# Optimization experiments

Measured on AMD Instinct MI355X. Metric: run time of the kernel, lower is better.

Reference implementation:

```python
import jax, jax.numpy as jnp
import numpy as np

N_NODES = 100000


def gcn_conv(x, edge_index, W, b, n_nodes):
    """PyG GCNConv: add self-loops, symmetric deg^-1/2 normalization,
    linear transform, scatter-add aggregate, bias."""
    src, dst = edge_index[0], edge_index[1]
    # add self-loops
    loop = jnp.arange(n_nodes, dtype=edge_index.dtype)
    src = jnp.concatenate([src, loop])
    dst = jnp.concatenate([dst, loop])
    # transform first (in_dim >= out_dim ordering used by PyG)
    h = x @ W  # [N, out]
    # symmetric normalization from in-degree (incl. self-loops)
    ones = jnp.ones(src.shape[0], dtype=x.dtype)
    deg = jax.ops.segment_sum(ones, dst, num_segments=n_nodes)
    dinv = jnp.where(deg > 0, jax.lax.rsqrt(deg), 0.0).astype(x.dtype)
    norm = dinv[src] * dinv[dst]  # [E+N]
    msg = h[src] * norm[:, None]  # gather + scale
    out = jax.ops.segment_sum(msg, dst, num_segments=n_nodes)
    return out + b


def setup_inputs() -> dict:
    key = jax.random.key(0)
    k1, k2, k3, k4 = jax.random.split(key, 4)
    n, e = N_NODES, 1600000
    d_in, d_hid, n_cls = 256, 256, 64
    x = jax.random.normal(k1, (n, d_in), dtype=jnp.float32)
    edge_index = jax.random.randint(k2, (2, e), 0, n, dtype=jnp.int64)
    W1 = jax.random.normal(k3, (d_in, d_hid), dtype=jnp.float32) / np.sqrt(d_in)
    b1 = jnp.zeros((d_hid,), dtype=jnp.float32)
    W2 = jax.random.normal(k4, (d_hid, n_cls), dtype=jnp.float32) / np.sqrt(d_hid)
    b2 = jnp.zeros((n_cls,), dtype=jnp.float32)
    return {"x": x, "edge_index": edge_index, "W1": W1, "b1": b1, "W2": W2, "b2": b2}


def reference(x, edge_index, W1, b1, W2, b2):
    n = x.shape[0]
    h = jax.nn.relu(gcn_conv(x, edge_index, W1, b1, n))
    # dropout is identity in eval mode (training=False)
    logits = gcn_conv(h, edge_index, W2, b2, n)
    return jax.nn.log_softmax(logits, axis=1)
```

## Files before the change

kernel.cpp:

```cpp
#include <hip/hip_runtime.h>
#include <math.h>


typedef __attribute__((ext_vector_type(8))) short bf16x8;
typedef __attribute__((ext_vector_type(4))) float f32x4;

__device__ inline unsigned short f2bf(float f) {
    union { float f; unsigned int u; } v; v.f = f;
    unsigned int r = v.u + 0x7fffu + ((v.u >> 16) & 1u);
    return (unsigned short)(r >> 16);
}
__device__ inline float bf2f_lo(unsigned int u) {
    union { unsigned int u; float f; } v; v.u = u << 16; return v.f;
}
__device__ inline float bf2f_hi(unsigned int u) {
    union { unsigned int u; float f; } v; v.u = u & 0xffff0000u; return v.f;
}

__device__ inline void acc8(float* acc, uint4 q, float w) {
    acc[0] += bf2f_lo(q.x) * w; acc[1] += bf2f_hi(q.x) * w;
    acc[2] += bf2f_lo(q.y) * w; acc[3] += bf2f_hi(q.y) * w;
    acc[4] += bf2f_lo(q.z) * w; acc[5] += bf2f_hi(q.z) * w;
    acc[6] += bf2f_lo(q.w) * w; acc[7] += bf2f_hi(q.w) * w;
}

__global__ __launch_bounds__(256) void deg_rank_kernel(
    const int* __restrict__ dst, int E, int* __restrict__ cnt,
    int* __restrict__ rank) {
    int e = blockIdx.x * blockDim.x + threadIdx.x;
    if (e < E) rank[e] = atomicAdd(&cnt[dst[e]], 1);
}

__global__ __launch_bounds__(256) void scan_part1_kernel(
    const int* __restrict__ cnt, int* __restrict__ bsum, int N) {
    __shared__ int s[256];
    const int tid = threadIdx.x;
    int base = blockIdx.x * 1024 + tid * 4;
    int v = 0;
#pragma unroll
    for (int j = 0; j < 4; ++j)
        if (base + j < N) v += cnt[base + j];
    s[tid] = v;
    __syncthreads();
    for (int off = 128; off > 0; off >>= 1) {
        if (tid < off) s[tid] += s[tid + off];
        __syncthreads();
    }
    if (tid == 0) bsum[blockIdx.x] = s[0];
}

__global__ __launch_bounds__(1024) void scan_part2_kernel(
    const int* __restrict__ bsum, int* __restrict__ boffs, int NB,
    int* __restrict__ row_ptr, int N) {
    __shared__ int s[1024];
    const int tid = threadIdx.x;
    int v = (tid < NB) ? bsum[tid] : 0;
    s[tid] = v;
    __syncthreads();
    for (int off = 1; off < 1024; off <<= 1) {
        int t = (tid >= off) ? s[tid - off] : 0;
        __syncthreads();
        if (tid >= off) s[tid] += t;
        __syncthreads();
    }
    if (tid < NB) boffs[tid] = s[tid] - v;
    if (tid == 1023) row_ptr[N] = s[1023];
}

__global__ __launch_bounds__(256) void scan_part3_kernel(
    const int* __restrict__ cnt, const int* __restrict__ boffs,
    int* __restrict__ row_ptr, int N) {
    __shared__ int s[256];
    const int tid = threadIdx.x;
    int base = blockIdx.x * 1024 + tid * 4;
    int c[4];
    int v = 0;
#pragma unroll
    for (int j = 0; j < 4; ++j) {
        c[j] = (base + j < N) ? cnt[base + j] : 0;
        v += c[j];
    }
    s[tid] = v;
    __syncthreads();
    for (int off = 1; off < 256; off <<= 1) {
        int t = (tid >= off) ? s[tid - off] : 0;
        __syncthreads();
        if (tid >= off) s[tid] += t;
        __syncthreads();
    }
    int run = boffs[blockIdx.x] + s[tid] - v;
#pragma unroll
    for (int j = 0; j < 4; ++j) {
        if (base + j < N) {
            row_ptr[base + j] = run;
            run += c[j];
        }
    }
}

__global__ __launch_bounds__(256) void scatter_kernel(
    const int* __restrict__ src, const int* __restrict__ dst,
    const int* __restrict__ rank, const int* __restrict__ cnt,
    const int* __restrict__ row_ptr, int2* __restrict__ csr_ew, int E) {
    int e = blockIdx.x * blockDim.x + threadIdx.x;
    if (e >= E) return;
    int s = src[e], d = dst[e];
    float w = rsqrtf((float)cnt[s] + 1.0f) * rsqrtf((float)cnt[d] + 1.0f);
    int pos = row_ptr[d] + rank[e];
    int2 rec;
    rec.x = s;
    rec.y = __float_as_int(w);
    csr_ew[pos] = rec;
}

__global__ __launch_bounds__(256) void castw_kernel(
    const float* __restrict__ W1, const float* __restrict__ W2,
    unsigned short* __restrict__ W1t, unsigned short* __restrict__ W2t) {
    int i = blockIdx.x * 256 + threadIdx.x;
    if (i < 65536) {
        int n = i >> 8, k = i & 255;
        W1t[i] = f2bf(W1[(size_t)k * 256 + n]);
    } else if (i < 65536 + 16384) {
        int j = i - 65536;
        int n = j >> 8, k = j & 255;
        W2t[j] = f2bf(W2[(size_t)k * 64 + n]);
    }
}

__global__ __launch_bounds__(256) void gemm1_kernel(
    const float* __restrict__ A, const unsigned short* __restrict__ Bt,
    unsigned short* __restrict__ C, int M) {
    __shared__ unsigned short As[128][32];
    __shared__ unsigned short Bs[256][32];

    const int tid = threadIdx.x;
    const int wave = tid >> 6, lane = tid & 63;
    const int quad = lane >> 4, l15 = lane & 15;
    const int m0 = blockIdx.x * 128;

    f32x4 acc[8][4] = {};

    const int arow = tid >> 1;
    const int akk  = (tid & 1) << 4;
    const int gr = m0 + arow;

    for (int k0 = 0; k0 < 256; k0 += 32) {
        float4 a0 = make_float4(0.f,0.f,0.f,0.f), a1 = a0, a2 = a0, a3 = a0;
        if (gr < M) {
            const float* ap = &A[(size_t)gr * 256 + k0 + akk];
            a0 = *(const float4*)&ap[0];
            a1 = *(const float4*)&ap[4];
            a2 = *(const float4*)&ap[8];
            a3 = *(const float4*)&ap[12];
        }
        bf16x8 av0, av1;
        av0[0] = (short)f2bf(a0.x); av0[1] = (short)f2bf(a0.y);
        av0[2] = (short)f2bf(a0.z); av0[3] = (short)f2bf(a0.w);
        av0[4] = (short)f2bf(a1.x); av0[5] = (short)f2bf(a1.y);
        av0[6] = (short)f2bf(a1.z); av0[7] = (short)f2bf(a1.w);
        av1[0] = (short)f2bf(a2.x); av1[1] = (short)f2bf(a2.y);
        av1[2] = (short)f2bf(a2.z); av1[3] = (short)f2bf(a2.w);
        av1[4] = (short)f2bf(a3.x); av1[5] = (short)f2bf(a3.y);
        av1[6] = (short)f2bf(a3.z); av1[7] = (short)f2bf(a3.w);
        *(bf16x8*)&As[arow][akk]     = av0;
        *(bf16x8*)&As[arow][akk + 8] = av1;

        const unsigned short* bsrc = &Bt[(size_t)tid * 256 + k0];
        *(bf16x8*)&Bs[tid][0]  = *(const bf16x8*)&bsrc[0];
        *(bf16x8*)&Bs[tid][8]  = *(const bf16x8*)&bsrc[8];
        *(bf16x8*)&Bs[tid][16] = *(const bf16x8*)&bsrc[16];
        *(bf16x8*)&Bs[tid][24] = *(const bf16x8*)&bsrc[24];
        __syncthreads();

        bf16x8 bfv[4];
#pragma unroll
        for (int nt = 0; nt < 4; ++nt)
            bfv[nt] = *(const bf16x8*)&Bs[wave * 64 + nt * 16 + l15][quad * 8];
#pragma unroll
        for (int mt = 0; mt < 8; ++mt) {
            bf16x8 af = *(const bf16x8*)&As[mt * 16 + l15][quad * 8];
#pragma unroll
            for (int nt = 0; nt < 4; ++nt)
                acc[mt][nt] = __builtin_amdgcn_mfma_f32_16x16x32_bf16(
                    af, bfv[nt], acc[mt][nt], 0, 0, 0);
        }
        __syncthreads();
    }

#pragma unroll
    for (int mt = 0; mt < 8; ++mt) {
#pragma unroll
        for (int nt = 0; nt < 4; ++nt) {
            int gcol = wave * 64 + nt * 16 + l15;
#pragma unroll
            for (int r = 0; r < 4; ++r) {
                int grow = m0 + mt * 16 + quad * 4 + r;
                if (grow < M)
                    C[(size_t)grow * 256 + gcol] = f2bf(acc[mt][nt][r]);
            }
        }
    }
}

__global__ __launch_bounds__(256) void agg256b_kernel(
    const uint4* __restrict__ h,
    const int2* __restrict__ ew,
    const int* __restrict__ row_ptr, const int* __restrict__ cnt,
    const float* __restrict__ bias, uint4* __restrict__ outb, int N) {
    const int node = blockIdx.x * 4 + (threadIdx.x >> 6);
    if (node >= N) return;
    const int lane = threadIdx.x & 63;
    const int half = lane >> 5;
    const int c = lane & 31;

    float dv = rsqrtf((float)cnt[node] + 1.0f);
    float w0 = dv * dv;

    float acc[8] = {0.f, 0.f, 0.f, 0.f, 0.f, 0.f, 0.f, 0.f};
    {
        uint4 q = h[(size_t)node * 32 + c];
        acc8(acc, q, half == 0 ? w0 : 0.f);
    }

    const int beg = row_ptr[node], end = row_ptr[node + 1];
    int e = beg;
    for (; e + 8 <= end; e += 8) {
        int2 r0 = ew[e + 0 + half];
        int2 r1 = ew[e + 2 + half];
        int2 r2 = ew[e + 4 + half];
        int2 r3 = ew[e + 6 + half];
        uint4 q0 = h[(size_t)r0.x * 32 + c];
        uint4 q1 = h[(size_t)r1.x * 32 + c];
        uint4 q2 = h[(size_t)r2.x * 32 + c];
        uint4 q3 = h[(size_t)r3.x * 32 + c];
        acc8(acc, q0, __int_as_float(r0.y));
        acc8(acc, q1, __int_as_float(r1.y));
        acc8(acc, q2, __int_as_float(r2.y));
        acc8(acc, q3, __int_as_float(r3.y));
    }
    for (; e < end; e += 2) {
        int idx = e + half;
        int idxc = min(idx, end - 1);
        int2 r = ew[idxc];
        float w = (idx < end) ? __int_as_float(r.y) : 0.f;
        uint4 q = h[(size_t)r.x * 32 + c];
        acc8(acc, q, w);
    }

#pragma unroll
    for (int k = 0; k < 8; ++k) acc[k] += __shfl_xor(acc[k], 32, 64);

    if (half == 0) {
        float4 b0 = *(const float4*)&bias[c * 8];
        float4 b1 = *(const float4*)&bias[c * 8 + 4];
        unsigned int o0 = f2bf(fmaxf(acc[0] + b0.x, 0.f));
        unsigned int o1 = f2bf(fmaxf(acc[1] + b0.y, 0.f));
        unsigned int o2 = f2bf(fmaxf(acc[2] + b0.z, 0.f));
        unsigned int o3 = f2bf(fmaxf(acc[3] + b0.w, 0.f));
        unsigned int o4 = f2bf(fmaxf(acc[4] + b1.x, 0.f));
        unsigned int o5 = f2bf(fmaxf(acc[5] + b1.y, 0.f));
        unsigned int o6 = f2bf(fmaxf(acc[6] + b1.z, 0.f));
        unsigned int o7 = f2bf(fmaxf(acc[7] + b1.w, 0.f));
        uint4 ov;
        ov.x = o0 | (o1 << 16);
        ov.y = o2 | (o3 << 16);
        ov.z = o4 | (o5 << 16);
        ov.w = o6 | (o7 << 16);
        outb[(size_t)node * 32 + c] = ov;
    }
}

__global__ __launch_bounds__(256) void gemm2_kernel(
    const unsigned short* __restrict__ Ab, const unsigned short* __restrict__ Bt,
    unsigned short* __restrict__ C, int M) {
    __shared__ unsigned short As[64][32];
    __shared__ unsigned short Bs[64][32];

    const int tid = threadIdx.x;
    const int wave = tid >> 6, lane = tid & 63;
    const int quad = lane >> 4, l15 = lane & 15;
    const int m0 = blockIdx.x * 64;

    f32x4 acc[4] = {};

    const int arow = tid >> 2;
    const int akk = (tid & 3) << 3;
    const int gr = m0 + arow;
    const int bn = tid & 63, bkc = (tid >> 6) << 3;

    for (int k0 = 0; k0 < 256; k0 += 32) {
        bf16x8 av = {};
        if (gr < M) av = *(const bf16x8*)&Ab[(size_t)gr * 256 + k0 + akk];
        *(bf16x8*)&As[arow][akk] = av;
        *(bf16x8*)&Bs[bn][bkc] = *(const bf16x8*)&Bt[(size_t)bn * 256 + k0 + bkc];
        __syncthreads();

        bf16x8 af = *(const bf16x8*)&As[wave * 16 + l15][quad * 8];
#pragma unroll
        for (int nt = 0; nt < 4; ++nt) {
            bf16x8 bfv = *(const bf16x8*)&Bs[nt * 16 + l15][quad * 8];
            acc[nt] = __builtin_amdgcn_mfma_f32_16x16x32_bf16(af, bfv, acc[nt], 0, 0, 0);
        }
        __syncthreads();
    }

#pragma unroll
    for (int nt = 0; nt < 4; ++nt) {
#pragma unroll
        for (int r = 0; r < 4; ++r) {
            int grow = m0 + wave * 16 + quad * 4 + r;
            if (grow < M) C[(size_t)grow * 64 + nt * 16 + l15] = f2bf(acc[nt][r]);
        }
    }
}

__global__ __launch_bounds__(256) void agg64_kernel(
    const uint4* __restrict__ h,
    const int2* __restrict__ ew, const int* __restrict__ row_ptr,
    const int* __restrict__ cnt, const float* __restrict__ bias,
    float* __restrict__ out, int N) {
    const int node = blockIdx.x * 4 + (threadIdx.x >> 6);
    if (node >= N) return;
    const int lane = threadIdx.x & 63;
    const int g = lane >> 3;
    const int c = lane & 7;

    float dv = rsqrtf((float)cnt[node] + 1.0f);
    float w0 = dv * dv;

    float acc[8] = {0.f, 0.f, 0.f, 0.f, 0.f, 0.f, 0.f, 0.f};
    {
        uint4 q = h[(size_t)node * 8 + c];
        acc8(acc, q, g == 0 ? w0 : 0.f);
    }

    const int beg = row_ptr[node], end = row_ptr[node + 1];
    int e = beg;
    for (; e + 16 <= end; e += 16) {
        int2 r0 = ew[e + g];
        int2 r1 = ew[e + 8 + g];
        uint4 q0 = h[(size_t)r0.x * 8 + c];
        uint4 q1 = h[(size_t)r1.x * 8 + c];
        acc8(acc, q0, __int_as_float(r0.y));
        acc8(acc, q1, __int_as_float(r1.y));
    }
    for (; e < end; e += 8) {
        int idx = e + g;
        int idxc = min(idx, end - 1);
        int2 r = ew[idxc];
        float w = (idx < end) ? __int_as_float(r.y) : 0.f;
        uint4 q = h[(size_t)r.x * 8 + c];
        acc8(acc, q, w);
    }

#pragma unroll
    for (int k = 0; k < 8; ++k) {
        acc[k] += __shfl_xor(acc[k], 8, 64);
        acc[k] += __shfl_xor(acc[k], 16, 64);
        acc[k] += __shfl_xor(acc[k], 32, 64);
    }

    float4 b0 = *(const float4*)&bias[c * 8];
    float4 b1 = *(const float4*)&bias[c * 8 + 4];
    float v[8];
    v[0] = acc[0] + b0.x; v[1] = acc[1] + b0.y;
    v[2] = acc[2] + b0.z; v[3] = acc[3] + b0.w;
    v[4] = acc[4] + b1.x; v[5] = acc[5] + b1.y;
    v[6] = acc[6] + b1.z; v[7] = acc[7] + b1.w;

    float m = v[0];
#pragma unroll
    for (int k = 1; k < 8; ++k) m = fmaxf(m, v[k]);
    m = fmaxf(m, __shfl_xor(m, 1, 64));
    m = fmaxf(m, __shfl_xor(m, 2, 64));
    m = fmaxf(m, __shfl_xor(m, 4, 64));
    float s = 0.f;
#pragma unroll
    for (int k = 0; k < 8; ++k) s += expf(v[k] - m);
    s += __shfl_xor(s, 1, 64);
    s += __shfl_xor(s, 2, 64);
    s += __shfl_xor(s, 4, 64);
    float ls = m + logf(s);

    if (g == 0) {
        float4 o0, o1;
        o0.x = v[0] - ls; o0.y = v[1] - ls; o0.z = v[2] - ls; o0.w = v[3] - ls;
        o1.x = v[4] - ls; o1.y = v[5] - ls; o1.z = v[6] - ls; o1.w = v[7] - ls;
        *(float4*)&out[(size_t)node * 64 + c * 8] = o0;
        *(float4*)&out[(size_t)node * 64 + c * 8 + 4] = o1;
    }
}

extern "C" void kernel_launch(void* const* d_in, const int* in_sizes, int n_in,
                              void* d_out, int out_size, void* d_ws, size_t ws_size,
                              hipStream_t stream) {
    const float* x  = (const float*)d_in[0];
    const int*   ei = (const int*)d_in[1];
    const float* W1 = (const float*)d_in[2];
    const float* b1 = (const float*)d_in[3];
    const float* W2 = (const float*)d_in[4];
    const float* b2 = (const float*)d_in[5];
    float* out = (float*)d_out;

    const int N = in_sizes[0] / 256;
    const int E = in_sizes[1] / 2;
    const int NP = 102400;
    const int NB = (N + 1023) / 1024;

    char* ws = (char*)d_ws;
    int*   cnt     = (int*)ws;                 ws += (size_t)NP * 4;
    int*   rank    = (int*)ws;                 ws += (size_t)E * 4;
    int*   row_ptr = (int*)ws;                 ws += (size_t)(NP + 4) * 4;
    int*   bsum    = (int*)ws;                 ws += (size_t)1024 * 4;
    int*   boffs   = (int*)ws;                 ws += (size_t)1024 * 4;
    int2*  csr_ew  = (int2*)ws;                ws += (size_t)E * 8;
    unsigned short* W1t   = (unsigned short*)ws; ws += (size_t)256 * 256 * 2;
    unsigned short* W2t   = (unsigned short*)ws; ws += (size_t)256 * 64 * 2;
    unsigned short* h1b   = (unsigned short*)ws; ws += (size_t)N * 256 * 2;
    unsigned short* agg1b = (unsigned short*)ws; ws += (size_t)N * 256 * 2;
    unsigned short* h2b   = (unsigned short*)ws; ws += (size_t)N * 64 * 2;

    hipMemsetAsync(cnt, 0, (size_t)N * sizeof(int), stream);

    deg_rank_kernel<<<(E + 255) / 256, 256, 0, stream>>>(ei + E, E, cnt, rank);
    scan_part1_kernel<<<NB, 256, 0, stream>>>(cnt, bsum, N);
    scan_part2_kernel<<<1, 1024, 0, stream>>>(bsum, boffs, NB, row_ptr, N);
    scan_part3_kernel<<<NB, 256, 0, stream>>>(cnt, boffs, row_ptr, N);
    scatter_kernel<<<(E + 255) / 256, 256, 0, stream>>>(
        ei, ei + E, rank, cnt, row_ptr, csr_ew, E);

    castw_kernel<<<(65536 + 16384 + 255) / 256, 256, 0, stream>>>(W1, W2, W1t, W2t);

    gemm1_kernel<<<(N + 127) / 128, 256, 0, stream>>>(x, W1t, h1b, N);

    agg256b_kernel<<<(N + 3) / 4, 256, 0, stream>>>(
        (const uint4*)h1b, csr_ew, row_ptr, cnt, b1, (uint4*)agg1b, N);

    gemm2_kernel<<<(N + 63) / 64, 256, 0, stream>>>(agg1b, W2t, h2b, N);

    agg64_kernel<<<(N + 3) / 4, 256, 0, stream>>>(
        (const uint4*)h2b, csr_ew, row_ptr, cnt, b2, out, N);
}
```

Before: 554.4 us.

## Fuse layer-1 aggregation with layer-2 GEMM via shared-memory tile

The layer-1 neighbour aggregation kernel and the second GEMM become one kernel. Each block aggregates 16 nodes (4 per wave), applies bias and ReLU, stores the bf16 rows in LDS, then multiplies them by W2 with MFMA and writes h2 directly. This removes the N×256 bf16 intermediate write/read and one launch. In exchange each wave processes 4 nodes serially and W2t fragments are read from global memory per block, not staged in LDS.

```diff
diff --git a/kernel.cpp b/kernel.cpp
--- a/kernel.cpp
+++ b/kernel.cpp
@@ -202,115 +202,94 @@
     }
 }
 
-__global__ __launch_bounds__(256) void agg256b_kernel(
+__global__ __launch_bounds__(256) void aggfused_kernel(
     const uint4* __restrict__ h,
     const int2* __restrict__ ew,
     const int* __restrict__ row_ptr, const int* __restrict__ cnt,
-    const float* __restrict__ bias, uint4* __restrict__ outb, int N) {
-    const int node = blockIdx.x * 4 + (threadIdx.x >> 6);
-    if (node >= N) return;
-    const int lane = threadIdx.x & 63;
+    const float* __restrict__ bias, const unsigned short* __restrict__ W2t,
+    unsigned short* __restrict__ h2b, int N) {
+    __shared__ unsigned short As[16][264];
+
+    const int tid = threadIdx.x;
+    const int wave = tid >> 6, lane = tid & 63;
     const int half = lane >> 5;
     const int c = lane & 31;
-
-    float dv = rsqrtf((float)cnt[node] + 1.0f);
-    float w0 = dv * dv;
-
-    float acc[8] = {0.f, 0.f, 0.f, 0.f, 0.f, 0.f, 0.f, 0.f};
-    {
-        uint4 q = h[(size_t)node * 32 + c];
-        acc8(acc, q, half == 0 ? w0 : 0.f);
-    }
-
-    const int beg = row_ptr[node], end = row_ptr[node + 1];
-    int e = beg;
-    for (; e + 8 <= end; e += 8) {
-        int2 r0 = ew[e + 0 + half];
-        int2 r1 = ew[e + 2 + half];
-        int2 r2 = ew[e + 4 + half];
-        int2 r3 = ew[e + 6 + half];
-        uint4 q0 = h[(size_t)r0.x * 32 + c];
-        uint4 q1 = h[(size_t)r1.x * 32 + c];
-        uint4 q2 = h[(size_t)r2.x * 32 + c];
-        uint4 q3 = h[(size_t)r3.x * 32 + c];
-        acc8(acc, q0, __int_as_float(r0.y));
-        acc8(acc, q1, __int_as_float(r1.y));
-        acc8(acc, q2, __int_as_float(r2.y));
-        acc8(acc, q3, __int_as_float(r3.y));
-    }
-    for (; e < end; e += 2) {
-        int idx = e + half;
-        int idxc = min(idx, end - 1);
-        int2 r = ew[idxc];
-        float w = (idx < end) ? __int_as_float(r.y) : 0.f;
-        uint4 q = h[(size_t)r.x * 32 + c];
-        acc8(acc, q, w);
-    }
-
-#pragma unroll
-    for (int k = 0; k < 8; ++k) acc[k] += __shfl_xor(acc[k], 32, 64);
-
-    if (half == 0) {
-        float4 b0 = *(const float4*)&bias[c * 8];
-        float4 b1 = *(const float4*)&bias[c * 8 + 4];
-        unsigned int o0 = f2bf(fmaxf(acc[0] + b0.x, 0.f));
-        unsigned int o1 = f2bf(fmaxf(acc[1] + b0.y, 0.f));
-        unsigned int o2 = f2bf(fmaxf(acc[2] + b0.z, 0.f));
-        unsigned int o3 = f2bf(fmaxf(acc[3] + b0.w, 0.f));
-        unsigned int o4 = f2bf(fmaxf(acc[4] + b1.x, 0.f));
-        unsigned int o5 = f2bf(fmaxf(acc[5] + b1.y, 0.f));
-        unsigned int o6 = f2bf(fmaxf(acc[6] + b1.z, 0.f));
-        unsigned int o7 = f2bf(fmaxf(acc[7] + b1.w, 0.f));
-        uint4 ov;
-        ov.x = o0 | (o1 << 16);
-        ov.y = o2 | (o3 << 16);
-        ov.z = o4 | (o5 << 16);
-        ov.w = o6 | (o7 << 16);
-        outb[(size_t)node * 32 + c] = ov;
-    }
-}
-
-__global__ __launch_bounds__(256) void gemm2_kernel(
-    const unsigned short* __restrict__ Ab, const unsigned short* __restrict__ Bt,
-    unsigned short* __restrict__ C, int M) {
-    __shared__ unsigned short As[64][32];
-    __shared__ unsigned short Bs[64][32];
-
-    const int tid = threadIdx.x;
-    const int wave = tid >> 6, lane = tid & 63;
+    const int node0 = blockIdx.x * 16;
+
+    for (int i = 0; i < 4; ++i) {
+        const int local = wave * 4 + i;
+        const int node = node0 + local;
+        float acc[8] = {0.f, 0.f, 0.f, 0.f, 0.f, 0.f, 0.f, 0.f};
+        if (node < N) {
+            float dv = rsqrtf((float)cnt[node] + 1.0f);
+            float w0 = dv * dv;
+            {
+                uint4 q = h[(size_t)node * 32 + c];
+                acc8(acc, q, half == 0 ? w0 : 0.f);
+            }
+            const int beg = row_ptr[node], end = row_ptr[node + 1];
+            int e = beg;
+            for (; e + 8 <= end; e += 8) {
+                int2 r0 = ew[e + 0 + half];
+                int2 r1 = ew[e + 2 + half];
+                int2 r2 = ew[e + 4 + half];
+                int2 r3 = ew[e + 6 + half];
+                uint4 q0 = h[(size_t)r0.x * 32 + c];
+                uint4 q1 = h[(size_t)r1.x * 32 + c];
+                uint4 q2 = h[(size_t)r2.x * 32 + c];
+                uint4 q3 = h[(size_t)r3.x * 32 + c];
+                acc8(acc, q0, __int_as_float(r0.y));
+                acc8(acc, q1, __int_as_float(r1.y));
+                acc8(acc, q2, __int_as_float(r2.y));
+                acc8(acc, q3, __int_as_float(r3.y));
+            }
+            for (; e < end; e += 2) {
+                int idx = e + half;
+                int idxc = min(idx, end - 1);
+                int2 r = ew[idxc];
+                float w = (idx < end) ? __int_as_float(r.y) : 0.f;
+                uint4 q = h[(size_t)r.x * 32 + c];
+                acc8(acc, q, w);
+            }
+        }
+#pragma unroll
+        for (int k = 0; k < 8; ++k) acc[k] += __shfl_xor(acc[k], 32, 64);
+
+        if (half == 0) {
+            float4 b0 = *(const float4*)&bias[c * 8];
+            float4 b1 = *(const float4*)&bias[c * 8 + 4];
+            unsigned int o0 = f2bf(fmaxf(acc[0] + b0.x, 0.f));
+            unsigned int o1 = f2bf(fmaxf(acc[1] + b0.y, 0.f));
+            unsigned int o2 = f2bf(fmaxf(acc[2] + b0.z, 0.f));
+            unsigned int o3 = f2bf(fmaxf(acc[3] + b0.w, 0.f));
+            unsigned int o4 = f2bf(fmaxf(acc[4] + b1.x, 0.f));
+            unsigned int o5 = f2bf(fmaxf(acc[5] + b1.y, 0.f));
+            unsigned int o6 = f2bf(fmaxf(acc[6] + b1.z, 0.f));
+            unsigned int o7 = f2bf(fmaxf(acc[7] + b1.w, 0.f));
+            uint4 ov;
+            ov.x = o0 | (o1 << 16);
+            ov.y = o2 | (o3 << 16);
+            ov.z = o4 | (o5 << 16);
+            ov.w = o6 | (o7 << 16);
+            *(uint4*)&As[local][c * 8] = ov;
+        }
+    }
+    __syncthreads();
+
     const int quad = lane >> 4, l15 = lane & 15;
-    const int m0 = blockIdx.x * 64;
-
-    f32x4 acc[4] = {};
-
-    const int arow = tid >> 2;
-    const int akk = (tid & 3) << 3;
-    const int gr = m0 + arow;
-    const int bn = tid & 63, bkc = (tid >> 6) << 3;
-
-    for (int k0 = 0; k0 < 256; k0 += 32) {
-        bf16x8 av = {};
-        if (gr < M) av = *(const bf16x8*)&Ab[(size_t)gr * 256 + k0 + akk];
-        *(bf16x8*)&As[arow][akk] = av;
-        *(bf16x8*)&Bs[bn][bkc] = *(const bf16x8*)&Bt[(size_t)bn * 256 + k0 + bkc];
-        __syncthreads();
-
-        bf16x8 af = *(const bf16x8*)&As[wave * 16 + l15][quad * 8];
-#pragma unroll
-        for (int nt = 0; nt < 4; ++nt) {
-            bf16x8 bfv = *(const bf16x8*)&Bs[nt * 16 + l15][quad * 8];
-            acc[nt] = __builtin_amdgcn_mfma_f32_16x16x32_bf16(af, bfv, acc[nt], 0, 0, 0);
-        }
-        __syncthreads();
-    }
-
-#pragma unroll
-    for (int nt = 0; nt < 4; ++nt) {
-#pragma unroll
-        for (int r = 0; r < 4; ++r) {
-            int grow = m0 + wave * 16 + quad * 4 + r;
-            if (grow < M) C[(size_t)grow * 64 + nt * 16 + l15] = f2bf(acc[nt][r]);
-        }
+    f32x4 accd = {};
+#pragma unroll
+    for (int k0 = 0; k0 < 8; ++k0) {
+        bf16x8 af = *(const bf16x8*)&As[l15][k0 * 32 + quad * 8];
+        bf16x8 bf = *(const bf16x8*)&W2t[(size_t)(wave * 16 + l15) * 256 +
+                                         k0 * 32 + quad * 8];
+        accd = __builtin_amdgcn_mfma_f32_16x16x32_bf16(af, bf, accd, 0, 0, 0);
+    }
+#pragma unroll
+    for (int r = 0; r < 4; ++r) {
+        int node = node0 + quad * 4 + r;
+        if (node < N)
+            h2b[(size_t)node * 64 + wave * 16 + l15] = f2bf(accd[r]);
     }
 }
 
@@ -417,7 +396,6 @@
     unsigned short* W1t   = (unsigned short*)ws; ws += (size_t)256 * 256 * 2;
     unsigned short* W2t   = (unsigned short*)ws; ws += (size_t)256 * 64 * 2;
     unsigned short* h1b   = (unsigned short*)ws; ws += (size_t)N * 256 * 2;
-    unsigned short* agg1b = (unsigned short*)ws; ws += (size_t)N * 256 * 2;
     unsigned short* h2b   = (unsigned short*)ws; ws += (size_t)N * 64 * 2;
 
     hipMemsetAsync(cnt, 0, (size_t)N * sizeof(int), stream);
@@ -433,10 +411,8 @@
 
     gemm1_kernel<<<(N + 127) / 128, 256, 0, stream>>>(x, W1t, h1b, N);
 
-    agg256b_kernel<<<(N + 3) / 4, 256, 0, stream>>>(
-        (const uint4*)h1b, csr_ew, row_ptr, cnt, b1, (uint4*)agg1b, N);
-
-    gemm2_kernel<<<(N + 63) / 64, 256, 0, stream>>>(agg1b, W2t, h2b, N);
+    aggfused_kernel<<<(N + 15) / 16, 256, 0, stream>>>(
+        (const uint4*)h1b, csr_ew, row_ptr, cnt, b1, W2t, h2b, N);
 
     agg64_kernel<<<(N + 3) / 4, 256, 0, stream>>>(
         (const uint4*)h2b, csr_ew, row_ptr, cnt, b2, out, N);
```

After: 543.5 us. -2.0%, faster.
